# Optimization experiments

Hardware: AMD Instinct MI355X
Metric: run time of the kernel (lower is better)

## Reference

```python
import jax, jax.numpy as jnp
import numpy as np

SEQ_LEN = 512
INPUT_DIM = 128
HIDDEN_DIM = 2 * INPUT_DIM
N_FEATURES = 1
BATCH = 256


def _lstm_layer(x, W_ih, W_hh, b_ih, b_hh):
    # x: [B, S, D_in]; W_ih: [4H, D_in]; W_hh: [4H, H]; PyTorch gate order i,f,g,o
    B = x.shape[0]
    H = W_hh.shape[1]
    # precompute input projections for all timesteps: [S, B, 4H]
    x_proj = jnp.einsum('bsd,gd->sbg', x, W_ih) + b_ih + b_hh

    def step(carry, xt):
        h, c = carry
        gates = xt + h @ W_hh.T  # [B, 4H]
        i, f, g, o = jnp.split(gates, 4, axis=-1)
        i = jax.nn.sigmoid(i)
        f = jax.nn.sigmoid(f)
        g = jnp.tanh(g)
        o = jax.nn.sigmoid(o)
        c = f * c + i * g
        h = o * jnp.tanh(c)
        return (h, c), h

    h0 = jnp.zeros((B, H), dtype=x.dtype)
    c0 = jnp.zeros((B, H), dtype=x.dtype)
    _, hs = jax.lax.scan(step, (h0, c0), x_proj)  # hs: [S, B, H]
    return jnp.transpose(hs, (1, 0, 2))  # [B, S, H]


def setup_inputs() -> dict:
    key = jax.random.key(0)
    ks = jax.random.split(key, 11)
    s1 = 1.0 / np.sqrt(INPUT_DIM)
    s2 = 1.0 / np.sqrt(HIDDEN_DIM)
    return {
        'x': jax.random.normal(ks[0], (BATCH, INPUT_DIM), dtype=jnp.float32),
        'W_ih1': jax.random.uniform(ks[1], (4 * INPUT_DIM, INPUT_DIM), minval=-s1, maxval=s1, dtype=jnp.float32),
        'W_hh1': jax.random.uniform(ks[2], (4 * INPUT_DIM, INPUT_DIM), minval=-s1, maxval=s1, dtype=jnp.float32),
        'b_ih1': jax.random.uniform(ks[3], (4 * INPUT_DIM,), minval=-s1, maxval=s1, dtype=jnp.float32),
        'b_hh1': jax.random.uniform(ks[4], (4 * INPUT_DIM,), minval=-s1, maxval=s1, dtype=jnp.float32),
        'W_ih2': jax.random.uniform(ks[5], (4 * HIDDEN_DIM, INPUT_DIM), minval=-s2, maxval=s2, dtype=jnp.float32),
        'W_hh2': jax.random.uniform(ks[6], (4 * HIDDEN_DIM, HIDDEN_DIM), minval=-s2, maxval=s2, dtype=jnp.float32),
        'b_ih2': jax.random.uniform(ks[7], (4 * HIDDEN_DIM,), minval=-s2, maxval=s2, dtype=jnp.float32),
        'b_hh2': jax.random.uniform(ks[8], (4 * HIDDEN_DIM,), minval=-s2, maxval=s2, dtype=jnp.float32),
        'W_out': jax.random.uniform(ks[9], (N_FEATURES, HIDDEN_DIM), minval=-s2, maxval=s2, dtype=jnp.float32),
        'b_out': jax.random.uniform(ks[10], (N_FEATURES,), minval=-s2, maxval=s2, dtype=jnp.float32),
    }


def reference(x, W_ih1, W_hh1, b_ih1, b_hh1, W_ih2, W_hh2, b_ih2, b_hh2, W_out, b_out):
    # repeat latent over time: [B, S, input_dim]
    xt = jnp.broadcast_to(x[:, None, :], (x.shape[0], SEQ_LEN, x.shape[1]))
    h1 = _lstm_layer(xt, W_ih1, W_hh1, b_ih1, b_hh1)   # [B, S, input_dim]
    h2 = _lstm_layer(h1, W_ih2, W_hh2, b_ih2, b_hh2)   # [B, S, 2*input_dim]
    return h2 @ W_out.T + b_out                         # [B, S, n_features]
```

## Files before the change

### kernel.cpp

```cpp
#include <hip/hip_runtime.h>

#define S 512
#define B 256
#define D 128
#define H1 128
#define H2 256

#define NGRP 8
#define BG 32
#define WPG 10
#define NWG 80
#define GRP_FLAGS 10

#define OFF_XPROJ 0u
#define OFF_H1HI  524288u
#define OFF_H1LO  655360u
#define OFF_H2HI  786432u
#define OFF_H2LO  1048576u
#define OFF_OUTP  1310720u
#define OFF_FLAG  5505024u

#define DYN_LDS 67072

typedef unsigned long long ull;
typedef unsigned short ushort;
typedef __attribute__((ext_vector_type(8))) short short8;
typedef __attribute__((ext_vector_type(4))) float f32x4;

__device__ __forceinline__ ushort f2bf(float f){
  unsigned u = __float_as_uint(f);
  unsigned r = u + 0x7fffu + ((u>>16)&1u);
  return (ushort)(r>>16);
}
__device__ __forceinline__ float rcpf_(float x){ return __builtin_amdgcn_rcpf(x); }
__device__ __forceinline__ float sigm(float x){ return rcpf_(1.f + __expf(-x)); }
__device__ __forceinline__ float tanh_(float x){ return 1.f - 2.f*rcpf_(1.f + __expf(2.f*x)); }

__device__ __forceinline__ void ast8(ull* p, ull v){
  __hip_atomic_store(p, v, __ATOMIC_RELAXED, __HIP_MEMORY_SCOPE_AGENT);
}
__device__ __forceinline__ ull ald8(const ull* p){
  return __hip_atomic_load(p, __ATOMIC_RELAXED, __HIP_MEMORY_SCOPE_AGENT);
}
__device__ __forceinline__ ull pk4(ushort a, ushort b, ushort c, ushort d){
  return (ull)a | ((ull)b<<16) | ((ull)c<<32) | ((ull)d<<48);
}

__global__ void k_zero(char* wsb){
  long long id = (long long)blockIdx.x*blockDim.x + threadIdx.x;
  long long stride = (long long)gridDim.x*blockDim.x;
  ull* h = (ull*)(wsb + OFF_H1HI);
  for (long long i = id; i < 98304; i += stride) h[i] = 0ull;
  ull* f = (ull*)(wsb + OFF_FLAG);
  for (long long i = id; i < 128; i += stride) f[i] = 0ull;
}

__global__ void k_xproj(const float* __restrict__ x, const float* __restrict__ Wih1,
                        const float* __restrict__ bih1, const float* __restrict__ bhh1,
                        char* __restrict__ wsb){
  __shared__ float xs[D];
  float* xproj = (float*)(wsb + OFF_XPROJ);
  int b = blockIdx.x;
  for (int d = threadIdx.x; d < D; d += blockDim.x) xs[d] = x[b*D + d];
  __syncthreads();
  for (int g = threadIdx.x; g < 4*H1; g += blockDim.x){
    float acc = bih1[g] + bhh1[g];
    const float* w = &Wih1[(size_t)g*D];
    #pragma unroll 8
    for (int d = 0; d < D; ++d) acc += xs[d]*w[d];
    xproj[(size_t)b*512 + g] = acc;
  }
}

__device__ __forceinline__ void wait_group(int* gf, int t, int need){
  if (t < 64){
    for(;;){
      int f = (t < GRP_FLAGS)
        ? __hip_atomic_load(&gf[t], __ATOMIC_RELAXED, __HIP_MEMORY_SCOPE_AGENT)
        : 0x7fffffff;
      if (__all(f >= need)) break;
      __builtin_amdgcn_s_sleep(1);
    }
  }
  __syncthreads();
}
__device__ __forceinline__ void flag_done(int* gf, int slot, int t, int r){
  __syncthreads();
  if (t == 0){
    __hip_atomic_store(&gf[slot], r+1, __ATOMIC_RELAXED, __HIP_MEMORY_SCOPE_AGENT);
  }
}

__global__ void __launch_bounds__(256,1)
k_persist(const float* __restrict__ Whh1,
          const float* __restrict__ Wih2, const float* __restrict__ Whh2,
          const float* __restrict__ bih2, const float* __restrict__ bhh2,
          const float* __restrict__ Wout,
          char* __restrict__ wsb){
  extern __shared__ char sm[];
  const int wg = blockIdx.x;
  const int t  = threadIdx.x;
  const int grp = wg / WPG, role = wg % WPG;
  const int gb0 = grp * BG;
  const int l = t & 63, wv = t >> 6, lr = l & 15, lk = (l >> 4) * 8;

  float* xproj = (float*)(wsb + OFF_XPROJ);
  ull* h1hi = (ull*)(wsb + OFF_H1HI);
  ull* h1lo = (ull*)(wsb + OFF_H1LO);
  ull* h2hi = (ull*)(wsb + OFF_H2HI);
  ull* h2lo = (ull*)(wsb + OFF_H2LO);
  float* outp = (float*)(wsb + OFF_OUTP);
  int* gf = (int*)(wsb + OFF_FLAG) + grp*32;

  if (role < 2){
    const int u0 = role * 64;
    ushort* hsH = (ushort*)sm;
    ushort* hsL = (ushort*)(sm + 8704);
    float*  gl  = (float*)(sm + 17408);

    short8 bhi[4][4], blo[4][4];
    #pragma unroll
    for (int kt=0;kt<4;++kt){
      #pragma unroll
      for (int ct=0;ct<4;++ct){
        int col = wv*64 + ct*16 + lr;
        int lu = col>>2, g = col&3;
        const float* src = Whh1 + (size_t)(g*H1 + u0 + lu)*D + kt*32 + lk;
        short8 vh, vl;
        #pragma unroll
        for (int j=0;j<8;++j){
          float w = src[j];
          ushort hb = f2bf(w);
          float hf = __uint_as_float((unsigned)hb<<16);
          vh[j] = (short)hb; vl[j] = (short)f2bf(w - hf);
        }
        bhi[kt][ct]=vh; blo[kt][ct]=vl;
      }
    }
    f32x4 xpf[2][4];
    #pragma unroll
    for (int bt=0;bt<2;++bt){
      #pragma unroll
      for (int ct=0;ct<4;++ct){
        int col = wv*64 + ct*16 + lr;
        int lu = col>>2, g = col&3;
        #pragma unroll
        for (int q=0;q<4;++q){
          int b = gb0 + bt*16 + (l>>4)*4 + q;
          xpf[bt][ct][q] = xproj[(size_t)b*512 + g*H1 + u0 + lu];
        }
      }
    }
    const int nb = t>>3, lu0 = (t&7)*8;
    float c1[8];
    #pragma unroll
    for (int j=0;j<8;++j) c1[j]=0.f;

    for (int r=0; r<=S; ++r){
      if (r>0) wait_group(gf, t, r);
      if (r<S){
        const int pr = (r+1)&1, pw = r&1;
        const ull* sH = h1hi + (size_t)pr*8192;
        const ull* sL = h1lo + (size_t)pr*8192;
        ull tH[4], tL[4];
        #pragma unroll
        for (int m=0;m<4;++m){
          int id = t + m*256;
          int b = id>>5, k4 = id&31;
          size_t go = (size_t)(gb0+b)*32 + k4;
          tH[m] = ald8(sH+go);
          tL[m] = ald8(sL+go);
        }
        #pragma unroll
        for (int m=0;m<4;++m){
          int id = t + m*256;
          int b = id>>5, k4 = id&31;
          *(ull*)(hsH + b*136 + k4*4) = tH[m];
          *(ull*)(hsL + b*136 + k4*4) = tL[m];
        }
        __syncthreads();
        f32x4 acc[2][4];
        #pragma unroll
        for (int bt=0;bt<2;++bt){
          #pragma unroll
          for (int ct=0;ct<4;++ct) acc[bt][ct]=xpf[bt][ct];
        }
        #pragma unroll
        for (int kt=0;kt<4;++kt){
          short8 ah[2], al[2];
          #pragma unroll
          for (int bt=0;bt<2;++bt){
            int off = (bt*16+lr)*136 + kt*32 + lk;
            ah[bt] = *(const short8*)(hsH + off);
            al[bt] = *(const short8*)(hsL + off);
          }
          #pragma unroll
          for (int bt=0;bt<2;++bt){
            #pragma unroll
            for (int ct=0;ct<4;++ct){
              acc[bt][ct] = __builtin_amdgcn_mfma_f32_16x16x32_bf16(ah[bt], bhi[kt][ct], acc[bt][ct],0,0,0);
              acc[bt][ct] = __builtin_amdgcn_mfma_f32_16x16x32_bf16(al[bt], bhi[kt][ct], acc[bt][ct],0,0,0);
              acc[bt][ct] = __builtin_amdgcn_mfma_f32_16x16x32_bf16(ah[bt], blo[kt][ct], acc[bt][ct],0,0,0);
            }
          }
        }
        #pragma unroll
        for (int bt=0;bt<2;++bt){
          #pragma unroll
          for (int ct=0;ct<4;++ct){
            #pragma unroll
            for (int q=0;q<4;++q)
              gl[(bt*16 + (l>>4)*4 + q)*260 + wv*64 + ct*16 + lr] = acc[bt][ct][q];
          }
        }
        __syncthreads();
        float hv[8];
        #pragma unroll
        for (int j=0;j<8;++j){
          f32x4 gv = *(const f32x4*)&gl[nb*260 + (lu0+j)*4];
          float ig = sigm(gv[0]), fg = sigm(gv[1]);
          float gg = tanh_(gv[2]), og = sigm(gv[3]);
          c1[j] = fg*c1[j] + ig*gg;
          hv[j] = og*tanh_(c1[j]);
        }
        ushort hb[8], lb[8];
        #pragma unroll
        for (int j=0;j<8;++j){
          hb[j] = f2bf(hv[j]);
          float hf = __uint_as_float((unsigned)hb[j]<<16);
          lb[j] = f2bf(hv[j]-hf);
        }
        size_t db = (size_t)pw*8192 + (size_t)(gb0+nb)*32 + ((u0+lu0)>>2);
        ast8(h1hi+db,   pk4(hb[0],hb[1],hb[2],hb[3]));
        ast8(h1hi+db+1, pk4(hb[4],hb[5],hb[6],hb[7]));
        ast8(h1lo+db,   pk4(lb[0],lb[1],lb[2],lb[3]));
        ast8(h1lo+db+1, pk4(lb[4],lb[5],lb[6],lb[7]));
      }
      flag_done(gf, role, t, r);
    }
  } else {
    const int us = role - 2;
    const int u0 = us * 32;
    ushort* hcH = (ushort*)sm;
    ushort* hcL = (ushort*)(sm + 25088);
    float*  gl  = (float*)(sm + 50176);

    short8 bhi[12][2], blo[12][2];
    #pragma unroll
    for (int kt=0;kt<12;++kt){
      #pragma unroll
      for (int ct=0;ct<2;++ct){
        int col = wv*32 + ct*16 + lr;
        int lu = col>>2, g = col&3;
        int row = g*H2 + u0 + lu;
        const float* src = (kt<4) ? (Wih2 + (size_t)row*D + kt*32 + lk)
                                  : (Whh2 + (size_t)row*H2 + (kt-4)*32 + lk);
        short8 vh, vl;
        #pragma unroll
        for (int j=0;j<8;++j){
          float w = src[j];
          ushort hb = f2bf(w);
          float hf = __uint_as_float((unsigned)hb<<16);
          vh[j] = (short)hb; vl[j] = (short)f2bf(w - hf);
        }
        bhi[kt][ct]=vh; blo[kt][ct]=vl;
      }
    }
    float biasv[2];
    #pragma unroll
    for (int ct=0;ct<2;++ct){
      int col = wv*32 + ct*16 + lr;
      int lu = col>>2, g = col&3;
      biasv[ct] = bih2[g*H2+u0+lu] + bhh2[g*H2+u0+lu];
    }
    const int nb = t>>3, lu0 = (t&7)*4;
    float wo[4];
    #pragma unroll
    for (int j=0;j<4;++j) wo[j] = Wout[u0+lu0+j];
    float c2[4] = {0.f,0.f,0.f,0.f};

    for (int r=0; r<=S; ++r){
      if (r>0) wait_group(gf, t, r);
      if (r>=1){
        const int ts = r-1;
        const int p1 = (r-1)&1;
        const int p2r = r&1, p2w = (r-1)&1;
        const ull* s1H = h1hi + (size_t)p1*8192;
        const ull* s1L = h1lo + (size_t)p1*8192;
        const ull* s2H = h2hi + (size_t)p2r*16384;
        const ull* s2L = h2lo + (size_t)p2r*16384;
        ull t1H[4], t1L[4], t2H[8], t2L[8];
        #pragma unroll
        for (int m=0;m<4;++m){
          int id = t + m*256;
          int b = id>>5, s = id&31;
          size_t go = (size_t)(gb0+b)*32 + s;
          t1H[m] = ald8(s1H+go);
          t1L[m] = ald8(s1L+go);
        }
        #pragma unroll
        for (int m=0;m<8;++m){
          int id = t + m*256;
          int b = id>>6, s = id&63;
          size_t go = (size_t)(gb0+b)*64 + s;
          t2H[m] = ald8(s2H+go);
          t2L[m] = ald8(s2L+go);
        }
        #pragma unroll
        for (int m=0;m<4;++m){
          int id = t + m*256;
          int b = id>>5, s = id&31;
          *(ull*)(hcH + b*392 + s*4) = t1H[m];
          *(ull*)(hcL + b*392 + s*4) = t1L[m];
        }
        #pragma unroll
        for (int m=0;m<8;++m){
          int id = t + m*256;
          int b = id>>6, s = id&63;
          *(ull*)(hcH + b*392 + 128 + s*4) = t2H[m];
          *(ull*)(hcL + b*392 + 128 + s*4) = t2L[m];
        }
        __syncthreads();
        f32x4 acc[2][2];
        #pragma unroll
        for (int bt=0;bt<2;++bt){
          #pragma unroll
          for (int ct=0;ct<2;++ct){
            f32x4 a; a[0]=biasv[ct]; a[1]=biasv[ct]; a[2]=biasv[ct]; a[3]=biasv[ct];
            acc[bt][ct]=a;
          }
        }
        #pragma unroll
        for (int kt=0;kt<12;++kt){
          short8 ah[2], al[2];
          #pragma unroll
          for (int bt=0;bt<2;++bt){
            int off = (bt*16+lr)*392 + kt*32 + lk;
            ah[bt] = *(const short8*)(hcH + off);
            al[bt] = *(const short8*)(hcL + off);
          }
          #pragma unroll
          for (int bt=0;bt<2;++bt){
            #pragma unroll
            for (int ct=0;ct<2;++ct){
              acc[bt][ct] = __builtin_amdgcn_mfma_f32_16x16x32_bf16(ah[bt], bhi[kt][ct], acc[bt][ct],0,0,0);
              acc[bt][ct] = __builtin_amdgcn_mfma_f32_16x16x32_bf16(al[bt], bhi[kt][ct], acc[bt][ct],0,0,0);
              acc[bt][ct] = __builtin_amdgcn_mfma_f32_16x16x32_bf16(ah[bt], blo[kt][ct], acc[bt][ct],0,0,0);
            }
          }
        }
        #pragma unroll
        for (int bt=0;bt<2;++bt){
          #pragma unroll
          for (int ct=0;ct<2;++ct){
            #pragma unroll
            for (int q=0;q<4;++q)
              gl[(bt*16 + (l>>4)*4 + q)*132 + wv*32 + ct*16 + lr] = acc[bt][ct][q];
          }
        }
        __syncthreads();
        float psum = 0.f;
        ushort hb[4], lb[4];
        #pragma unroll
        for (int j=0;j<4;++j){
          f32x4 gv = *(const f32x4*)&gl[nb*132 + (lu0+j)*4];
          float ig = sigm(gv[0]), fg = sigm(gv[1]);
          float gg = tanh_(gv[2]), og = sigm(gv[3]);
          c2[j] = fg*c2[j] + ig*gg;
          float h = og*tanh_(c2[j]);
          psum += h*wo[j];
          hb[j] = f2bf(h);
          lb[j] = f2bf(h - __uint_as_float((unsigned)hb[j]<<16));
        }
        size_t db = (size_t)p2w*16384 + (size_t)(gb0+nb)*64 + ((u0+lu0)>>2);
        ast8(h2hi+db, pk4(hb[0],hb[1],hb[2],hb[3]));
        ast8(h2lo+db, pk4(lb[0],lb[1],lb[2],lb[3]));
        psum += __shfl_xor(psum,1,64);
        psum += __shfl_xor(psum,2,64);
        psum += __shfl_xor(psum,4,64);
        if ((t&7)==0) outp[(size_t)ts*2048 + us*256 + gb0+nb] = psum;
      }
      flag_done(gf, role, t, r);
    }
  }
}

__global__ void k_final(const char* __restrict__ wsb, const float* __restrict__ bout,
                        float* __restrict__ out){
  const float* outp = (const float*)(wsb + OFF_OUTP);
  int id = blockIdx.x*blockDim.x + threadIdx.x;
  if (id >= B*S) return;
  int tt = id >> 8;
  int b  = id & 255;
  float s = bout[0];
  const float* p = outp + (size_t)tt*2048 + b;
  #pragma unroll
  for (int u = 0; u < 8; ++u) s += p[(size_t)u*256];
  out[(size_t)b*S + tt] = s;
}

extern "C" void kernel_launch(void* const* d_in, const int* in_sizes, int n_in,
                              void* d_out, int out_size, void* d_ws, size_t ws_size,
                              hipStream_t stream){
  const float* x    = (const float*)d_in[0];
  const float* Wih1 = (const float*)d_in[1];
  const float* Whh1 = (const float*)d_in[2];
  const float* bih1 = (const float*)d_in[3];
  const float* bhh1 = (const float*)d_in[4];
  const float* Wih2 = (const float*)d_in[5];
  const float* Whh2 = (const float*)d_in[6];
  const float* bih2 = (const float*)d_in[7];
  const float* bhh2 = (const float*)d_in[8];
  const float* Wout = (const float*)d_in[9];
  const float* bout = (const float*)d_in[10];
  char* wsb  = (char*)d_ws;
  float* out = (float*)d_out;

  (void)hipFuncSetAttribute((const void*)k_persist,
                            hipFuncAttributeMaxDynamicSharedMemorySize, DYN_LDS);

  k_zero<<<dim3(64), dim3(256), 0, stream>>>(wsb);
  k_xproj<<<dim3(B), dim3(256), 0, stream>>>(x, Wih1, bih1, bhh1, wsb);
  k_persist<<<dim3(NWG), dim3(256), DYN_LDS, stream>>>(Whh1, Wih2, Whh2, bih2, bhh2, Wout, wsb);
  k_final<<<dim3((B*S)/256), dim3(256), 0, stream>>>(wsb, bout, out);
}
```

Before: 2.059 ms.

## Replace group-wide lockstep barrier with per-wave tags and quad-buffered hidden states

Each workgroup used to publish one flag per step after a block barrier, and every workgroup in a group waited on all of them, which kept layer 1 and layer 2 in lockstep. Now each wave publishes its own tag after a vmcnt drain. The hidden-state buffers grow from double to quad buffering, so layer-1 workgroups can run up to two steps ahead of layer 2. Layer-2 workgroups wait on the layer-1 tags first and compute the input-projection MFMAs before waiting on the layer-2 tags. The cost is more flags to poll, a larger workspace, and memory-ordering risk from relying on relaxed atomics plus waitcnt.

```diff
diff --git a/kernel.cpp b/kernel.cpp
--- a/kernel.cpp
+++ b/kernel.cpp
@@ -10,15 +10,14 @@
 #define BG 32
 #define WPG 10
 #define NWG 80
-#define GRP_FLAGS 10
 
 #define OFF_XPROJ 0u
 #define OFF_H1HI  524288u
-#define OFF_H1LO  655360u
-#define OFF_H2HI  786432u
-#define OFF_H2LO  1048576u
-#define OFF_OUTP  1310720u
-#define OFF_FLAG  5505024u
+#define OFF_H1LO  786432u
+#define OFF_H2HI  1048576u
+#define OFF_H2LO  1572864u
+#define OFF_OUTP  2097152u
+#define OFF_TAGS  6291456u
 
 #define DYN_LDS 67072
 
@@ -42,6 +41,9 @@
 __device__ __forceinline__ ull ald8(const ull* p){
   return __hip_atomic_load(p, __ATOMIC_RELAXED, __HIP_MEMORY_SCOPE_AGENT);
 }
+__device__ __forceinline__ int aldi(const int* p){
+  return __hip_atomic_load(p, __ATOMIC_RELAXED, __HIP_MEMORY_SCOPE_AGENT);
+}
 __device__ __forceinline__ ull pk4(ushort a, ushort b, ushort c, ushort d){
   return (ull)a | ((ull)b<<16) | ((ull)c<<32) | ((ull)d<<48);
 }
@@ -50,9 +52,9 @@
   long long id = (long long)blockIdx.x*blockDim.x + threadIdx.x;
   long long stride = (long long)gridDim.x*blockDim.x;
   ull* h = (ull*)(wsb + OFF_H1HI);
-  for (long long i = id; i < 98304; i += stride) h[i] = 0ull;
-  ull* f = (ull*)(wsb + OFF_FLAG);
-  for (long long i = id; i < 128; i += stride) f[i] = 0ull;
+  for (long long i = id; i < 196608; i += stride) h[i] = 0ull;
+  ull* f = (ull*)(wsb + OFF_TAGS);
+  for (long long i = id; i < 256; i += stride) f[i] = 0ull;
 }
 
 __global__ void k_xproj(const float* __restrict__ x, const float* __restrict__ Wih1,
@@ -72,23 +74,31 @@
   }
 }
 
-__device__ __forceinline__ void wait_group(int* gf, int t, int need){
+__device__ __forceinline__ void wait_tags(const int* tags, int t, int lo, int hi, int need){
   if (t < 64){
     for(;;){
-      int f = (t < GRP_FLAGS)
-        ? __hip_atomic_load(&gf[t], __ATOMIC_RELAXED, __HIP_MEMORY_SCOPE_AGENT)
-        : 0x7fffffff;
+      int f = (t >= lo && t < hi) ? aldi(&tags[t]) : 0x7fffffff;
       if (__all(f >= need)) break;
       __builtin_amdgcn_s_sleep(1);
     }
   }
   __syncthreads();
 }
-__device__ __forceinline__ void flag_done(int* gf, int slot, int t, int r){
+__device__ __forceinline__ void wait_l1(const int* tags, int t, int r){
+  if (t < 64){
+    int need = (t < 8) ? r : (r-2);
+    for(;;){
+      int f = (t < 40) ? aldi(&tags[t]) : 0x7fffffff;
+      if (__all(f >= need)) break;
+      __builtin_amdgcn_s_sleep(1);
+    }
+  }
   __syncthreads();
-  if (t == 0){
-    __hip_atomic_store(&gf[slot], r+1, __ATOMIC_RELAXED, __HIP_MEMORY_SCOPE_AGENT);
-  }
+}
+__device__ __forceinline__ void publish(int* tags, int slot, int lane, int v){
+  asm volatile("s_waitcnt vmcnt(0)" ::: "memory");
+  if (lane == 0)
+    __hip_atomic_store(&tags[slot], v, __ATOMIC_RELAXED, __HIP_MEMORY_SCOPE_AGENT);
 }
 
 __global__ void __launch_bounds__(256,1)
@@ -110,13 +120,14 @@
   ull* h2hi = (ull*)(wsb + OFF_H2HI);
   ull* h2lo = (ull*)(wsb + OFF_H2LO);
   float* outp = (float*)(wsb + OFF_OUTP);
-  int* gf = (int*)(wsb + OFF_FLAG) + grp*32;
+  int* tags = (int*)(wsb + OFF_TAGS) + grp*64;
 
   if (role < 2){
     const int u0 = role * 64;
     ushort* hsH = (ushort*)sm;
     ushort* hsL = (ushort*)(sm + 8704);
     float*  gl  = (float*)(sm + 17408);
+    const int slot = role*4 + wv;
 
     short8 bhi[4][4], blo[4][4];
     #pragma unroll
@@ -156,12 +167,12 @@
     #pragma unroll
     for (int j=0;j<8;++j) c1[j]=0.f;
 
-    for (int r=0; r<=S; ++r){
-      if (r>0) wait_group(gf, t, r);
-      if (r<S){
-        const int pr = (r+1)&1, pw = r&1;
-        const ull* sH = h1hi + (size_t)pr*8192;
-        const ull* sL = h1lo + (size_t)pr*8192;
+    for (int r=0; r<S; ++r){
+      if (r>0) wait_l1(tags, t, r);
+      {
+        const int rb = (r-1)&3, wb = r&3;
+        const ull* sH = h1hi + (size_t)rb*8192;
+        const ull* sL = h1lo + (size_t)rb*8192;
         ull tH[4], tL[4];
         #pragma unroll
         for (int m=0;m<4;++m){
@@ -230,13 +241,13 @@
           float hf = __uint_as_float((unsigned)hb[j]<<16);
           lb[j] = f2bf(hv[j]-hf);
         }
-        size_t db = (size_t)pw*8192 + (size_t)(gb0+nb)*32 + ((u0+lu0)>>2);
+        size_t db = (size_t)wb*8192 + (size_t)(gb0+nb)*32 + ((u0+lu0)>>2);
         ast8(h1hi+db,   pk4(hb[0],hb[1],hb[2],hb[3]));
         ast8(h1hi+db+1, pk4(hb[4],hb[5],hb[6],hb[7]));
         ast8(h1lo+db,   pk4(lb[0],lb[1],lb[2],lb[3]));
         ast8(h1lo+db+1, pk4(lb[4],lb[5],lb[6],lb[7]));
+        publish(tags, slot, l, r+1);
       }
-      flag_done(gf, role, t, r);
     }
   } else {
     const int us = role - 2;
@@ -244,6 +255,7 @@
     ushort* hcH = (ushort*)sm;
     ushort* hcL = (ushort*)(sm + 25088);
     float*  gl  = (float*)(sm + 50176);
+    const int slot = 8 + us*4 + wv;
 
     short8 bhi[12][2], blo[12][2];
     #pragma unroll
@@ -280,16 +292,12 @@
     float c2[4] = {0.f,0.f,0.f,0.f};
 
     for (int r=0; r<=S; ++r){
-      if (r>0) wait_group(gf, t, r);
       if (r>=1){
         const int ts = r-1;
-        const int p1 = (r-1)&1;
-        const int p2r = r&1, p2w = (r-1)&1;
-        const ull* s1H = h1hi + (size_t)p1*8192;
-        const ull* s1L = h1lo + (size_t)p1*8192;
-        const ull* s2H = h2hi + (size_t)p2r*16384;
-        const ull* s2L = h2lo + (size_t)p2r*16384;
-        ull t1H[4], t1L[4], t2H[8], t2L[8];
+        wait_tags(tags, t, 0, 8, r);
+        const ull* s1H = h1hi + (size_t)((r-1)&3)*8192;
+        const ull* s1L = h1lo + (size_t)((r-1)&3)*8192;
+        ull t1H[4], t1L[4];
         #pragma unroll
         for (int m=0;m<4;++m){
           int id = t + m*256;
@@ -299,6 +307,46 @@
           t1L[m] = ald8(s1L+go);
         }
         #pragma unroll
+        for (int m=0;m<4;++m){
+          int id = t + m*256;
+          int b = id>>5, s = id&31;
+          *(ull*)(hcH + b*392 + s*4) = t1H[m];
+          *(ull*)(hcL + b*392 + s*4) = t1L[m];
+        }
+        __syncthreads();
+        f32x4 acc[2][2];
+        #pragma unroll
+        for (int bt=0;bt<2;++bt){
+          #pragma unroll
+          for (int ct=0;ct<2;++ct){
+            f32x4 a; a[0]=biasv[ct]; a[1]=biasv[ct]; a[2]=biasv[ct]; a[3]=biasv[ct];
+            acc[bt][ct]=a;
+          }
+        }
+        #pragma unroll
+        for (int kt=0;kt<4;++kt){
+          short8 ah[2], al[2];
+          #pragma unroll
+          for (int bt=0;bt<2;++bt){
+            int off = (bt*16+lr)*392 + kt*32 + lk;
+            ah[bt] = *(const short8*)(hcH + off);
+            al[bt] = *(const short8*)(hcL + off);
+          }
+          #pragma unroll
+          for (int bt=0;bt<2;++bt){
+            #pragma unroll
+            for (int ct=0;ct<2;++ct){
+              acc[bt][ct] = __builtin_amdgcn_mfma_f32_16x16x32_bf16(ah[bt], bhi[kt][ct], acc[bt][ct],0,0,0);
+              acc[bt][ct] = __builtin_amdgcn_mfma_f32_16x16x32_bf16(al[bt], bhi[kt][ct], acc[bt][ct],0,0,0);
+              acc[bt][ct] = __builtin_amdgcn_mfma_f32_16x16x32_bf16(ah[bt], blo[kt][ct], acc[bt][ct],0,0,0);
+            }
+          }
+        }
+        wait_tags(tags, t, 8, 40, r);
+        const ull* s2H = h2hi + (size_t)((r-2)&3)*16384;
+        const ull* s2L = h2lo + (size_t)((r-2)&3)*16384;
+        ull t2H[8], t2L[8];
+        #pragma unroll
         for (int m=0;m<8;++m){
           int id = t + m*256;
           int b = id>>6, s = id&63;
@@ -307,13 +355,6 @@
           t2L[m] = ald8(s2L+go);
         }
         #pragma unroll
-        for (int m=0;m<4;++m){
-          int id = t + m*256;
-          int b = id>>5, s = id&31;
-          *(ull*)(hcH + b*392 + s*4) = t1H[m];
-          *(ull*)(hcL + b*392 + s*4) = t1L[m];
-        }
-        #pragma unroll
         for (int m=0;m<8;++m){
           int id = t + m*256;
           int b = id>>6, s = id&63;
@@ -321,17 +362,8 @@
           *(ull*)(hcL + b*392 + 128 + s*4) = t2L[m];
         }
         __syncthreads();
-        f32x4 acc[2][2];
-        #pragma unroll
-        for (int bt=0;bt<2;++bt){
-          #pragma unroll
-          for (int ct=0;ct<2;++ct){
-            f32x4 a; a[0]=biasv[ct]; a[1]=biasv[ct]; a[2]=biasv[ct]; a[3]=biasv[ct];
-            acc[bt][ct]=a;
-          }
-        }
-        #pragma unroll
-        for (int kt=0;kt<12;++kt){
+        #pragma unroll
+        for (int kt=4;kt<12;++kt){
           short8 ah[2], al[2];
           #pragma unroll
           for (int bt=0;bt<2;++bt){
@@ -372,15 +404,17 @@
           hb[j] = f2bf(h);
           lb[j] = f2bf(h - __uint_as_float((unsigned)hb[j]<<16));
         }
-        size_t db = (size_t)p2w*16384 + (size_t)(gb0+nb)*64 + ((u0+lu0)>>2);
+        size_t db = (size_t)((r-1)&3)*16384 + (size_t)(gb0+nb)*64 + ((u0+lu0)>>2);
         ast8(h2hi+db, pk4(hb[0],hb[1],hb[2],hb[3]));
         ast8(h2lo+db, pk4(lb[0],lb[1],lb[2],lb[3]));
+        publish(tags, slot, l, r+1);
         psum += __shfl_xor(psum,1,64);
         psum += __shfl_xor(psum,2,64);
         psum += __shfl_xor(psum,4,64);
         if ((t&7)==0) outp[(size_t)ts*2048 + us*256 + gb0+nb] = psum;
+      } else {
+        publish(tags, slot, l, 1);
       }
-      flag_done(gf, role, t, r);
     }
   }
 }
```

Measured after the change: 2.472 ms. +20.1%, slower.

## Decouple LSTM layer-1 and layer-2 workgroups with 4-deep h buffers and lagged waits

Applied to the files above, without the earlier changes.

Replaces the lockstep group barrier, where every workgroup waited on every flag each round, with per-layer wait conditions. Layer-1 workgroups now wait only on their layer-1 peers for the current step and allow layer-2 to trail by up to two steps, using four-slot ring buffers for h1 and h2 instead of double buffers. Layer-2 signals its flag before doing the output-projection reduction, so that reduction is off the critical path. The aim is to let the layer-1 recurrence run ahead instead of being held back by the slower layer-2 step, at the cost of twice the workspace and more complex slot and flag bookkeeping.

```diff
diff --git a/kernel.cpp b/kernel.cpp
--- a/kernel.cpp
+++ b/kernel.cpp
@@ -10,15 +10,14 @@
 #define BG 32
 #define WPG 10
 #define NWG 80
-#define GRP_FLAGS 10
 
 #define OFF_XPROJ 0u
 #define OFF_H1HI  524288u
-#define OFF_H1LO  655360u
-#define OFF_H2HI  786432u
-#define OFF_H2LO  1048576u
-#define OFF_OUTP  1310720u
-#define OFF_FLAG  5505024u
+#define OFF_H1LO  786432u
+#define OFF_H2HI  1048576u
+#define OFF_H2LO  1572864u
+#define OFF_OUTP  2097152u
+#define OFF_FLAG  6291456u
 
 #define DYN_LDS 67072
 
@@ -42,6 +41,9 @@
 __device__ __forceinline__ ull ald8(const ull* p){
   return __hip_atomic_load(p, __ATOMIC_RELAXED, __HIP_MEMORY_SCOPE_AGENT);
 }
+__device__ __forceinline__ int aldi(const int* p){
+  return __hip_atomic_load(p, __ATOMIC_RELAXED, __HIP_MEMORY_SCOPE_AGENT);
+}
 __device__ __forceinline__ ull pk4(ushort a, ushort b, ushort c, ushort d){
   return (ull)a | ((ull)b<<16) | ((ull)c<<32) | ((ull)d<<48);
 }
@@ -50,9 +52,9 @@
   long long id = (long long)blockIdx.x*blockDim.x + threadIdx.x;
   long long stride = (long long)gridDim.x*blockDim.x;
   ull* h = (ull*)(wsb + OFF_H1HI);
-  for (long long i = id; i < 98304; i += stride) h[i] = 0ull;
+  for (long long i = id; i < 196608; i += stride) h[i] = 0ull;
   ull* f = (ull*)(wsb + OFF_FLAG);
-  for (long long i = id; i < 128; i += stride) f[i] = 0ull;
+  for (long long i = id; i < 256; i += stride) f[i] = 0ull;
 }
 
 __global__ void k_xproj(const float* __restrict__ x, const float* __restrict__ Wih1,
@@ -72,22 +74,31 @@
   }
 }
 
-__device__ __forceinline__ void wait_group(int* gf, int t, int need){
+__device__ __forceinline__ void wait_l1(const int* gf, int t, int r){
+  if (t < 64){
+    int need = (t < 2) ? r : (r-2);
+    for(;;){
+      int f = (t < 10) ? aldi(&gf[t]) : 0x7fffffff;
+      if (__all(f >= need)) break;
+      __builtin_amdgcn_s_sleep(1);
+    }
+  }
+  __syncthreads();
+}
+__device__ __forceinline__ void wait_l2(const int* gf, int t, int r){
   if (t < 64){
     for(;;){
-      int f = (t < GRP_FLAGS)
-        ? __hip_atomic_load(&gf[t], __ATOMIC_RELAXED, __HIP_MEMORY_SCOPE_AGENT)
-        : 0x7fffffff;
-      if (__all(f >= need)) break;
+      int f = (t < 10) ? aldi(&gf[t]) : 0x7fffffff;
+      if (__all(f >= r)) break;
       __builtin_amdgcn_s_sleep(1);
     }
   }
   __syncthreads();
 }
-__device__ __forceinline__ void flag_done(int* gf, int slot, int t, int r){
+__device__ __forceinline__ void flag_done(int* gf, int slot, int t, int v){
   __syncthreads();
   if (t == 0){
-    __hip_atomic_store(&gf[slot], r+1, __ATOMIC_RELAXED, __HIP_MEMORY_SCOPE_AGENT);
+    __hip_atomic_store(&gf[slot], v, __ATOMIC_RELAXED, __HIP_MEMORY_SCOPE_AGENT);
   }
 }
 
@@ -156,87 +167,85 @@
     #pragma unroll
     for (int j=0;j<8;++j) c1[j]=0.f;
 
-    for (int r=0; r<=S; ++r){
-      if (r>0) wait_group(gf, t, r);
-      if (r<S){
-        const int pr = (r+1)&1, pw = r&1;
-        const ull* sH = h1hi + (size_t)pr*8192;
-        const ull* sL = h1lo + (size_t)pr*8192;
-        ull tH[4], tL[4];
-        #pragma unroll
-        for (int m=0;m<4;++m){
-          int id = t + m*256;
-          int b = id>>5, k4 = id&31;
-          size_t go = (size_t)(gb0+b)*32 + k4;
-          tH[m] = ald8(sH+go);
-          tL[m] = ald8(sL+go);
-        }
-        #pragma unroll
-        for (int m=0;m<4;++m){
-          int id = t + m*256;
-          int b = id>>5, k4 = id&31;
-          *(ull*)(hsH + b*136 + k4*4) = tH[m];
-          *(ull*)(hsL + b*136 + k4*4) = tL[m];
-        }
-        __syncthreads();
-        f32x4 acc[2][4];
+    for (int r=0; r<S; ++r){
+      if (r>0) wait_l1(gf, t, r);
+      const int rb = (r-1)&3, wb = r&3;
+      const ull* sH = h1hi + (size_t)rb*8192;
+      const ull* sL = h1lo + (size_t)rb*8192;
+      ull tH[4], tL[4];
+      #pragma unroll
+      for (int m=0;m<4;++m){
+        int id = t + m*256;
+        int b = id>>5, k4 = id&31;
+        size_t go = (size_t)(gb0+b)*32 + k4;
+        tH[m] = ald8(sH+go);
+        tL[m] = ald8(sL+go);
+      }
+      #pragma unroll
+      for (int m=0;m<4;++m){
+        int id = t + m*256;
+        int b = id>>5, k4 = id&31;
+        *(ull*)(hsH + b*136 + k4*4) = tH[m];
+        *(ull*)(hsL + b*136 + k4*4) = tL[m];
+      }
+      __syncthreads();
+      f32x4 acc[2][4];
+      #pragma unroll
+      for (int bt=0;bt<2;++bt){
+        #pragma unroll
+        for (int ct=0;ct<4;++ct) acc[bt][ct]=xpf[bt][ct];
+      }
+      #pragma unroll
+      for (int kt=0;kt<4;++kt){
+        short8 ah[2], al[2];
         #pragma unroll
         for (int bt=0;bt<2;++bt){
-          #pragma unroll
-          for (int ct=0;ct<4;++ct) acc[bt][ct]=xpf[bt][ct];
-        }
-        #pragma unroll
-        for (int kt=0;kt<4;++kt){
-          short8 ah[2], al[2];
-          #pragma unroll
-          for (int bt=0;bt<2;++bt){
-            int off = (bt*16+lr)*136 + kt*32 + lk;
-            ah[bt] = *(const short8*)(hsH + off);
-            al[bt] = *(const short8*)(hsL + off);
-          }
-          #pragma unroll
-          for (int bt=0;bt<2;++bt){
-            #pragma unroll
-            for (int ct=0;ct<4;++ct){
-              acc[bt][ct] = __builtin_amdgcn_mfma_f32_16x16x32_bf16(ah[bt], bhi[kt][ct], acc[bt][ct],0,0,0);
-              acc[bt][ct] = __builtin_amdgcn_mfma_f32_16x16x32_bf16(al[bt], bhi[kt][ct], acc[bt][ct],0,0,0);
-              acc[bt][ct] = __builtin_amdgcn_mfma_f32_16x16x32_bf16(ah[bt], blo[kt][ct], acc[bt][ct],0,0,0);
-            }
-          }
+          int off = (bt*16+lr)*136 + kt*32 + lk;
+          ah[bt] = *(const short8*)(hsH + off);
+          al[bt] = *(const short8*)(hsL + off);
         }
         #pragma unroll
         for (int bt=0;bt<2;++bt){
           #pragma unroll
           for (int ct=0;ct<4;++ct){
-            #pragma unroll
-            for (int q=0;q<4;++q)
-              gl[(bt*16 + (l>>4)*4 + q)*260 + wv*64 + ct*16 + lr] = acc[bt][ct][q];
+            acc[bt][ct] = __builtin_amdgcn_mfma_f32_16x16x32_bf16(ah[bt], bhi[kt][ct], acc[bt][ct],0,0,0);
+            acc[bt][ct] = __builtin_amdgcn_mfma_f32_16x16x32_bf16(al[bt], bhi[kt][ct], acc[bt][ct],0,0,0);
+            acc[bt][ct] = __builtin_amdgcn_mfma_f32_16x16x32_bf16(ah[bt], blo[kt][ct], acc[bt][ct],0,0,0);
           }
         }
-        __syncthreads();
-        float hv[8];
-        #pragma unroll
-        for (int j=0;j<8;++j){
-          f32x4 gv = *(const f32x4*)&gl[nb*260 + (lu0+j)*4];
-          float ig = sigm(gv[0]), fg = sigm(gv[1]);
-          float gg = tanh_(gv[2]), og = sigm(gv[3]);
-          c1[j] = fg*c1[j] + ig*gg;
-          hv[j] = og*tanh_(c1[j]);
-        }
-        ushort hb[8], lb[8];
-        #pragma unroll
-        for (int j=0;j<8;++j){
-          hb[j] = f2bf(hv[j]);
-          float hf = __uint_as_float((unsigned)hb[j]<<16);
-          lb[j] = f2bf(hv[j]-hf);
-        }
-        size_t db = (size_t)pw*8192 + (size_t)(gb0+nb)*32 + ((u0+lu0)>>2);
-        ast8(h1hi+db,   pk4(hb[0],hb[1],hb[2],hb[3]));
-        ast8(h1hi+db+1, pk4(hb[4],hb[5],hb[6],hb[7]));
-        ast8(h1lo+db,   pk4(lb[0],lb[1],lb[2],lb[3]));
-        ast8(h1lo+db+1, pk4(lb[4],lb[5],lb[6],lb[7]));
-      }
-      flag_done(gf, role, t, r);
+      }
+      #pragma unroll
+      for (int bt=0;bt<2;++bt){
+        #pragma unroll
+        for (int ct=0;ct<4;++ct){
+          #pragma unroll
+          for (int q=0;q<4;++q)
+            gl[(bt*16 + (l>>4)*4 + q)*260 + wv*64 + ct*16 + lr] = acc[bt][ct][q];
+        }
+      }
+      __syncthreads();
+      float hv[8];
+      #pragma unroll
+      for (int j=0;j<8;++j){
+        f32x4 gv = *(const f32x4*)&gl[nb*260 + (lu0+j)*4];
+        float ig = sigm(gv[0]), fg = sigm(gv[1]);
+        float gg = tanh_(gv[2]), og = sigm(gv[3]);
+        c1[j] = fg*c1[j] + ig*gg;
+        hv[j] = og*tanh_(c1[j]);
+      }
+      ushort hb[8], lb[8];
+      #pragma unroll
+      for (int j=0;j<8;++j){
+        hb[j] = f2bf(hv[j]);
+        float hf = __uint_as_float((unsigned)hb[j]<<16);
+        lb[j] = f2bf(hv[j]-hf);
+      }
+      size_t db = (size_t)wb*8192 + (size_t)(gb0+nb)*32 + ((u0+lu0)>>2);
+      ast8(h1hi+db,   pk4(hb[0],hb[1],hb[2],hb[3]));
+      ast8(h1hi+db+1, pk4(hb[4],hb[5],hb[6],hb[7]));
+      ast8(h1lo+db,   pk4(lb[0],lb[1],lb[2],lb[3]));
+      ast8(h1lo+db+1, pk4(lb[4],lb[5],lb[6],lb[7]));
+      flag_done(gf, role, t, r+1);
     }
   } else {
     const int us = role - 2;
@@ -279,108 +288,108 @@
     for (int j=0;j<4;++j) wo[j] = Wout[u0+lu0+j];
     float c2[4] = {0.f,0.f,0.f,0.f};
 
-    for (int r=0; r<=S; ++r){
-      if (r>0) wait_group(gf, t, r);
-      if (r>=1){
-        const int ts = r-1;
-        const int p1 = (r-1)&1;
-        const int p2r = r&1, p2w = (r-1)&1;
-        const ull* s1H = h1hi + (size_t)p1*8192;
-        const ull* s1L = h1lo + (size_t)p1*8192;
-        const ull* s2H = h2hi + (size_t)p2r*16384;
-        const ull* s2L = h2lo + (size_t)p2r*16384;
-        ull t1H[4], t1L[4], t2H[8], t2L[8];
-        #pragma unroll
-        for (int m=0;m<4;++m){
-          int id = t + m*256;
-          int b = id>>5, s = id&31;
-          size_t go = (size_t)(gb0+b)*32 + s;
-          t1H[m] = ald8(s1H+go);
-          t1L[m] = ald8(s1L+go);
-        }
-        #pragma unroll
-        for (int m=0;m<8;++m){
-          int id = t + m*256;
-          int b = id>>6, s = id&63;
-          size_t go = (size_t)(gb0+b)*64 + s;
-          t2H[m] = ald8(s2H+go);
-          t2L[m] = ald8(s2L+go);
-        }
-        #pragma unroll
-        for (int m=0;m<4;++m){
-          int id = t + m*256;
-          int b = id>>5, s = id&31;
-          *(ull*)(hcH + b*392 + s*4) = t1H[m];
-          *(ull*)(hcL + b*392 + s*4) = t1L[m];
-        }
-        #pragma unroll
-        for (int m=0;m<8;++m){
-          int id = t + m*256;
-          int b = id>>6, s = id&63;
-          *(ull*)(hcH + b*392 + 128 + s*4) = t2H[m];
-          *(ull*)(hcL + b*392 + 128 + s*4) = t2L[m];
-        }
-        __syncthreads();
-        f32x4 acc[2][2];
+    for (int rr=0; rr<=S; ++rr){
+      if (rr == 0){
+        flag_done(gf, role, t, 1);
+        continue;
+      }
+      wait_l2(gf, t, rr);
+      const int ts = rr-1;
+      const ull* s1H = h1hi + (size_t)((rr-1)&3)*8192;
+      const ull* s1L = h1lo + (size_t)((rr-1)&3)*8192;
+      const ull* s2H = h2hi + (size_t)((rr-2)&3)*16384;
+      const ull* s2L = h2lo + (size_t)((rr-2)&3)*16384;
+      ull t1H[4], t1L[4], t2H[8], t2L[8];
+      #pragma unroll
+      for (int m=0;m<4;++m){
+        int id = t + m*256;
+        int b = id>>5, s = id&31;
+        size_t go = (size_t)(gb0+b)*32 + s;
+        t1H[m] = ald8(s1H+go);
+        t1L[m] = ald8(s1L+go);
+      }
+      #pragma unroll
+      for (int m=0;m<8;++m){
+        int id = t + m*256;
+        int b = id>>6, s = id&63;
+        size_t go = (size_t)(gb0+b)*64 + s;
+        t2H[m] = ald8(s2H+go);
+        t2L[m] = ald8(s2L+go);
+      }
+      #pragma unroll
+      for (int m=0;m<4;++m){
+        int id = t + m*256;
+        int b = id>>5, s = id&31;
+        *(ull*)(hcH + b*392 + s*4) = t1H[m];
+        *(ull*)(hcL + b*392 + s*4) = t1L[m];
+      }
+      #pragma unroll
+      for (int m=0;m<8;++m){
+        int id = t + m*256;
+        int b = id>>6, s = id&63;
+        *(ull*)(hcH + b*392 + 128 + s*4) = t2H[m];
+        *(ull*)(hcL + b*392 + 128 + s*4) = t2L[m];
+      }
+      __syncthreads();
+      f32x4 acc[2][2];
+      #pragma unroll
+      for (int bt=0;bt<2;++bt){
+        #pragma unroll
+        for (int ct=0;ct<2;++ct){
+          f32x4 a; a[0]=biasv[ct]; a[1]=biasv[ct]; a[2]=biasv[ct]; a[3]=biasv[ct];
+          acc[bt][ct]=a;
+        }
+      }
+      #pragma unroll
+      for (int kt=0;kt<12;++kt){
+        short8 ah[2], al[2];
+        #pragma unroll
+        for (int bt=0;bt<2;++bt){
+          int off = (bt*16+lr)*392 + kt*32 + lk;
+          ah[bt] = *(const short8*)(hcH + off);
+          al[bt] = *(const short8*)(hcL + off);
+        }
         #pragma unroll
         for (int bt=0;bt<2;++bt){
           #pragma unroll
           for (int ct=0;ct<2;++ct){
-            f32x4 a; a[0]=biasv[ct]; a[1]=biasv[ct]; a[2]=biasv[ct]; a[3]=biasv[ct];
-            acc[bt][ct]=a;
+            acc[bt][ct] = __builtin_amdgcn_mfma_f32_16x16x32_bf16(ah[bt], bhi[kt][ct], acc[bt][ct],0,0,0);
+            acc[bt][ct] = __builtin_amdgcn_mfma_f32_16x16x32_bf16(al[bt], bhi[kt][ct], acc[bt][ct],0,0,0);
+            acc[bt][ct] = __builtin_amdgcn_mfma_f32_16x16x32_bf16(ah[bt], blo[kt][ct], acc[bt][ct],0,0,0);
           }
         }
-        #pragma unroll
-        for (int kt=0;kt<12;++kt){
-          short8 ah[2], al[2];
+      }
+      #pragma unroll
+      for (int bt=0;bt<2;++bt){
+        #pragma unroll
+        for (int ct=0;ct<2;++ct){
           #pragma unroll
-          for (int bt=0;bt<2;++bt){
-            int off = (bt*16+lr)*392 + kt*32 + lk;
-            ah[bt] = *(const short8*)(hcH + off);
-            al[bt] = *(const short8*)(hcL + off);
-          }
-          #pragma unroll
-          for (int bt=0;bt<2;++bt){
-            #pragma unroll
-            for (int ct=0;ct<2;++ct){
-              acc[bt][ct] = __builtin_amdgcn_mfma_f32_16x16x32_bf16(ah[bt], bhi[kt][ct], acc[bt][ct],0,0,0);
-              acc[bt][ct] = __builtin_amdgcn_mfma_f32_16x16x32_bf16(al[bt], bhi[kt][ct], acc[bt][ct],0,0,0);
-              acc[bt][ct] = __builtin_amdgcn_mfma_f32_16x16x32_bf16(ah[bt], blo[kt][ct], acc[bt][ct],0,0,0);
-            }
-          }
-        }
-        #pragma unroll
-        for (int bt=0;bt<2;++bt){
-          #pragma unroll
-          for (int ct=0;ct<2;++ct){
-            #pragma unroll
-            for (int q=0;q<4;++q)
-              gl[(bt*16 + (l>>4)*4 + q)*132 + wv*32 + ct*16 + lr] = acc[bt][ct][q];
-          }
-        }
-        __syncthreads();
-        float psum = 0.f;
-        ushort hb[4], lb[4];
-        #pragma unroll
-        for (int j=0;j<4;++j){
-          f32x4 gv = *(const f32x4*)&gl[nb*132 + (lu0+j)*4];
-          float ig = sigm(gv[0]), fg = sigm(gv[1]);
-          float gg = tanh_(gv[2]), og = sigm(gv[3]);
-          c2[j] = fg*c2[j] + ig*gg;
-          float h = og*tanh_(c2[j]);
-          psum += h*wo[j];
-          hb[j] = f2bf(h);
-          lb[j] = f2bf(h - __uint_as_float((unsigned)hb[j]<<16));
-        }
-        size_t db = (size_t)p2w*16384 + (size_t)(gb0+nb)*64 + ((u0+lu0)>>2);
-        ast8(h2hi+db, pk4(hb[0],hb[1],hb[2],hb[3]));
-        ast8(h2lo+db, pk4(lb[0],lb[1],lb[2],lb[3]));
-        psum += __shfl_xor(psum,1,64);
-        psum += __shfl_xor(psum,2,64);
-        psum += __shfl_xor(psum,4,64);
-        if ((t&7)==0) outp[(size_t)ts*2048 + us*256 + gb0+nb] = psum;
-      }
-      flag_done(gf, role, t, r);
+          for (int q=0;q<4;++q)
+            gl[(bt*16 + (l>>4)*4 + q)*132 + wv*32 + ct*16 + lr] = acc[bt][ct][q];
+        }
+      }
+      __syncthreads();
+      float psum = 0.f;
+      ushort hb[4], lb[4];
+      #pragma unroll
+      for (int j=0;j<4;++j){
+        f32x4 gv = *(const f32x4*)&gl[nb*132 + (lu0+j)*4];
+        float ig = sigm(gv[0]), fg = sigm(gv[1]);
+        float gg = tanh_(gv[2]), og = sigm(gv[3]);
+        c2[j] = fg*c2[j] + ig*gg;
+        float h = og*tanh_(c2[j]);
+        psum += h*wo[j];
+        hb[j] = f2bf(h);
+        lb[j] = f2bf(h - __uint_as_float((unsigned)hb[j]<<16));
+      }
+      size_t db = (size_t)((rr-1)&3)*16384 + (size_t)(gb0+nb)*64 + ((u0+lu0)>>2);
+      ast8(h2hi+db, pk4(hb[0],hb[1],hb[2],hb[3]));
+      ast8(h2lo+db, pk4(lb[0],lb[1],lb[2],lb[3]));
+      flag_done(gf, role, t, rr+1);
+      psum += __shfl_xor(psum,1,64);
+      psum += __shfl_xor(psum,2,64);
+      psum += __shfl_xor(psum,4,64);
+      if ((t&7)==0) outp[(size_t)ts*2048 + us*256 + gb0+nb] = psum;
     }
   }
 }
```

After: 1.971 ms. 4.3% less time.
